# Performance work log

Measured on AMD Instinct MI355X. Metric: run time of the kernel, lower is better.

Reference implementation:

```python
import jax, jax.numpy as jnp
import numpy as np

B, C, H, W = 16, 192, 64, 64
L = 256           # number of quantization levels (len(sos.unique_values))
EXTREMA = 10.0    # codebook support roughly [-extrema, extrema]


def setup_inputs() -> dict:
    key = jax.random.key(0)
    k1, k2, k3 = jax.random.split(key, 3)
    inputs = jax.random.normal(k1, (B, C, H, W), dtype=jnp.float32) * 3.0
    means = jax.random.normal(k2, (B, C, H, W), dtype=jnp.float32)
    # sorted codebook of unique quantizer output values (sos.unique_values)
    raw = jax.random.uniform(k3, (L,), dtype=jnp.float32,
                             minval=-EXTREMA, maxval=EXTREMA)
    unique_values = jnp.sort(raw)
    return {"inputs": inputs, "means": means, "unique_values": unique_values}


def _nearest_symbols(v, unique_values):
    # Parallel binary search over the sorted codebook; equivalent to the
    # original per-element argmin(|keys - x|) in transform_map.
    L_ = unique_values.shape[0]
    idx = jnp.searchsorted(unique_values, v)          # in [0, L]
    idx = jnp.clip(idx, 1, L_ - 1)
    left = unique_values[idx - 1]
    right = unique_values[idx]
    # on ties, argmin picks the lower index -> use <=
    return jnp.where(jnp.abs(v - left) <= jnp.abs(v - right), idx - 1, idx)


def reference(inputs, means, unique_values):
    # quantize(mode='symbols'): subtract means, snap to nearest codebook
    # value, map value -> integer symbol via the sorted codebook.
    v = inputs - means
    symbols = _nearest_symbols(v, unique_values)      # int32 [B,C,H,W]
    # dequantize: symbol -> float codebook value (map_cdf_sos), add means.
    dequant = unique_values[symbols] + means          # float32 [B,C,H,W]
    return dequant, symbols
```

## Files before the change

### kernel.cpp

```cpp
#include <hip/hip_runtime.h>


#define LVL 256

__global__ __launch_bounds__(256) void agc_quant_kernel(
    const float* __restrict__ inputs,
    const float* __restrict__ means,
    const float* __restrict__ uv,
    float* __restrict__ out_deq,
    float* __restrict__ out_sym,
    int n4, int n)
{
    __shared__ float s_uv[LVL];
    s_uv[threadIdx.x] = uv[threadIdx.x];
    __syncthreads();

    int i = blockIdx.x * blockDim.x + threadIdx.x;
    if (i < n4) {
        float4 in = reinterpret_cast<const float4*>(inputs)[i];
        float4 mn = reinterpret_cast<const float4*>(means)[i];

        float vs[4] = {in.x - mn.x, in.y - mn.y, in.z - mn.z, in.w - mn.w};
        float ms[4] = {mn.x, mn.y, mn.z, mn.w};
        float dq[4], sy[4];

        #pragma unroll
        for (int k = 0; k < 4; ++k) {
            float v = vs[k];
            int lo = 0, hi = LVL;
            #pragma unroll
            for (int s = 0; s < 8; ++s) {
                int mid = (lo + hi) >> 1;
                bool go_right = (s_uv[mid] < v);
                lo = go_right ? (mid + 1) : lo;
                hi = go_right ? hi : mid;
            }
            int idx = min(max(lo, 1), LVL - 1);
            float left  = s_uv[idx - 1];
            float right = s_uv[idx];
            bool take_left = (fabsf(v - left) <= fabsf(v - right));
            int   sym = take_left ? (idx - 1) : idx;
            float val = take_left ? left : right;
            dq[k] = val + ms[k];
            sy[k] = (float)sym;
        }

        reinterpret_cast<float4*>(out_deq)[i] = make_float4(dq[0], dq[1], dq[2], dq[3]);
        reinterpret_cast<float4*>(out_sym)[i] = make_float4(sy[0], sy[1], sy[2], sy[3]);
    }

    if (blockIdx.x == 0 && threadIdx.x == 0) {
        for (int j = n4 * 4; j < n; ++j) {
            float m = means[j];
            float v = inputs[j] - m;
            int lo = 0, hi = LVL;
            for (int s = 0; s < 8; ++s) {
                int mid = (lo + hi) >> 1;
                bool go_right = (s_uv[mid] < v);
                lo = go_right ? (mid + 1) : lo;
                hi = go_right ? hi : mid;
            }
            int idx = min(max(lo, 1), LVL - 1);
            float left  = s_uv[idx - 1];
            float right = s_uv[idx];
            bool take_left = (fabsf(v - left) <= fabsf(v - right));
            int   sym = take_left ? (idx - 1) : idx;
            float val = take_left ? left : right;
            out_deq[j] = val + m;
            out_sym[j] = (float)sym;
        }
    }
}

extern "C" void kernel_launch(void* const* d_in, const int* in_sizes, int n_in,
                              void* d_out, int out_size, void* d_ws, size_t ws_size,
                              hipStream_t stream) {
    const float* inputs = (const float*)d_in[0];
    const float* means  = (const float*)d_in[1];
    const float* uv     = (const float*)d_in[2];

    int n  = in_sizes[0];
    int n4 = n / 4;

    float* out     = (float*)d_out;
    float* out_deq = out;
    float* out_sym = out + n;

    int threads = 256;
    int blocks  = (n4 + threads - 1) / threads;
    agc_quant_kernel<<<blocks, threads, 0, stream>>>(
        inputs, means, uv, out_deq, out_sym, n4, n);
}
```

Before: 180.4 us.

## Replace binary search with midpoint bucket lookup table and grid-stride loop

```diff
diff --git a/kernel.cpp b/kernel.cpp
--- a/kernel.cpp
+++ b/kernel.cpp
@@ -1,22 +1,76 @@
 #include <hip/hip_runtime.h>
 
 
-#define LVL 256
+#define LVL   256
+#define NMID  255
+#define MBUCK 4096
+
+
+__global__ __launch_bounds__(256) void agc_build_tables(
+    const float* __restrict__ uv, float* __restrict__ ws)
+{
+    __shared__ float s_uv[LVL];
+    __shared__ float s_mid[NMID];
+
+    int tid = threadIdx.x;
+    s_uv[tid] = uv[tid];
+    __syncthreads();
+
+    if (tid < NMID) {
+        float m = 0.5f * (s_uv[tid] + s_uv[tid + 1]);
+        s_mid[tid] = m;
+        ws[tid] = m;
+    }
+    __syncthreads();
+
+    float lo = s_mid[0];
+    float hi = s_mid[NMID - 1];
+    float scale = (hi > lo) ? ((float)MBUCK / (hi - lo)) : 0.0f;
+    float inv_scale = (hi > lo) ? ((hi - lo) / (float)MBUCK) : 0.0f;
+    if (tid == 0) { ws[256] = lo; ws[257] = scale; }
+
+    int* T = (int*)(ws + 512);
+    for (int m = tid; m < MBUCK; m += 256) {
+        float left = lo + (float)m * inv_scale;
+        int l = 0, h = NMID;
+        #pragma unroll
+        for (int s = 0; s < 8; ++s) {
+            int mid = (l + h) >> 1;
+            bool right = (s_mid[mid] < left);
+            l = right ? (mid + 1) : l;
+            h = right ? h : mid;
+        }
+        int b = l - 1;
+        T[m] = b < 0 ? 0 : b;
+    }
+}
 
 __global__ __launch_bounds__(256) void agc_quant_kernel(
     const float* __restrict__ inputs,
     const float* __restrict__ means,
     const float* __restrict__ uv,
+    const float* __restrict__ ws,
     float* __restrict__ out_deq,
     float* __restrict__ out_sym,
     int n4, int n)
 {
     __shared__ float s_uv[LVL];
-    s_uv[threadIdx.x] = uv[threadIdx.x];
+    __shared__ float s_mid[NMID + 1];
+    __shared__ int   s_T[MBUCK];
+
+    int tid = threadIdx.x;
+    s_uv[tid] = uv[tid];
+    if (tid < NMID) s_mid[tid] = ws[tid];
+    const int* gT = (const int*)(ws + 512);
+    #pragma unroll
+    for (int m = tid; m < MBUCK; m += 256) s_T[m] = gT[m];
+
+    float lo    = ws[256];
+    float scale = ws[257];
     __syncthreads();
 
-    int i = blockIdx.x * blockDim.x + threadIdx.x;
-    if (i < n4) {
+    int stride = gridDim.x * blockDim.x;
+    for (int i = blockIdx.x * blockDim.x + tid; i < n4; i += stride) {
         float4 in = reinterpret_cast<const float4*>(inputs)[i];
         float4 mn = reinterpret_cast<const float4*>(means)[i];
 
@@ -27,47 +81,30 @@
         #pragma unroll
         for (int k = 0; k < 4; ++k) {
             float v = vs[k];
-            int lo = 0, hi = LVL;
-            #pragma unroll
-            for (int s = 0; s < 8; ++s) {
-                int mid = (lo + hi) >> 1;
-                bool go_right = (s_uv[mid] < v);
-                lo = go_right ? (mid + 1) : lo;
-                hi = go_right ? hi : mid;
-            }
-            int idx = min(max(lo, 1), LVL - 1);
-            float left  = s_uv[idx - 1];
-            float right = s_uv[idx];
-            bool take_left = (fabsf(v - left) <= fabsf(v - right));
-            int   sym = take_left ? (idx - 1) : idx;
-            float val = take_left ? left : right;
-            dq[k] = val + ms[k];
-            sy[k] = (float)sym;
+            float f = (v - lo) * scale;
+            int m = (int)f;
+            m = m < 0 ? 0 : (m >= MBUCK ? MBUCK - 1 : m);
+            int base = s_T[m];
+            while (base < NMID && s_mid[base] < v) ++base;
+            sy[k] = (float)base;
+            dq[k] = s_uv[base] + ms[k];
         }
 
         reinterpret_cast<float4*>(out_deq)[i] = make_float4(dq[0], dq[1], dq[2], dq[3]);
         reinterpret_cast<float4*>(out_sym)[i] = make_float4(sy[0], sy[1], sy[2], sy[3]);
     }
 
-    if (blockIdx.x == 0 && threadIdx.x == 0) {
+    if (blockIdx.x == 0 && tid == 0) {
         for (int j = n4 * 4; j < n; ++j) {
-            float m = means[j];
-            float v = inputs[j] - m;
-            int lo = 0, hi = LVL;
-            for (int s = 0; s < 8; ++s) {
-                int mid = (lo + hi) >> 1;
-                bool go_right = (s_uv[mid] < v);
-                lo = go_right ? (mid + 1) : lo;
-                hi = go_right ? hi : mid;
-            }
-            int idx = min(max(lo, 1), LVL - 1);
-            float left  = s_uv[idx - 1];
-            float right = s_uv[idx];
-            bool take_left = (fabsf(v - left) <= fabsf(v - right));
-            int   sym = take_left ? (idx - 1) : idx;
-            float val = take_left ? left : right;
-            out_deq[j] = val + m;
-            out_sym[j] = (float)sym;
+            float mean = means[j];
+            float v = inputs[j] - mean;
+            float f = (v - lo) * scale;
+            int m = (int)f;
+            m = m < 0 ? 0 : (m >= MBUCK ? MBUCK - 1 : m);
+            int base = s_T[m];
+            while (base < NMID && s_mid[base] < v) ++base;
+            out_sym[j] = (float)base;
+            out_deq[j] = s_uv[base] + mean;
         }
     }
 }
@@ -85,9 +122,12 @@
     float* out     = (float*)d_out;
     float* out_deq = out;
     float* out_sym = out + n;
+    float* ws      = (float*)d_ws;
+
+    agc_build_tables<<<1, 256, 0, stream>>>(uv, ws);
 
     int threads = 256;
-    int blocks  = (n4 + threads - 1) / threads;
+    int blocks  = 1536;
     agc_quant_kernel<<<blocks, threads, 0, stream>>>(
-        inputs, means, uv, out_deq, out_sym, n4, n);
+        inputs, means, uv, ws, out_deq, out_sym, n4, n);
 }
```

Result: slower. 190.6 us (+5.7%).

## Replace per-element binary search with bucketed midpoint lookup table

Applied to the files above, without the earlier changes.

```diff
diff --git a/kernel.cpp b/kernel.cpp
--- a/kernel.cpp
+++ b/kernel.cpp
@@ -1,73 +1,156 @@
 #include <hip/hip_runtime.h>
+#include <math.h>
 
 
 #define LVL 256
 
-__global__ __launch_bounds__(256) void agc_quant_kernel(
-    const float* __restrict__ inputs,
-    const float* __restrict__ means,
-    const float* __restrict__ uv,
-    float* __restrict__ out_deq,
-    float* __restrict__ out_sym,
-    int n4, int n)
+__device__ __forceinline__ int lb_bj(const int* s_bj, int x) {
+    int lo = 0, hi = LVL;
+    #pragma unroll
+    for (int s = 0; s < 8; ++s) {
+        int mid = (lo + hi) >> 1;
+        bool r = (s_bj[mid] < x);
+        lo = r ? mid + 1 : lo;
+        hi = r ? hi : mid;
+    }
+    return lo;
+}
+
+__global__ __launch_bounds__(256) void agc_build(
+    const float* __restrict__ uv, float* __restrict__ ws, int NB)
 {
     __shared__ float s_uv[LVL];
-    s_uv[threadIdx.x] = uv[threadIdx.x];
+    __shared__ float s_mid[LVL];
+    __shared__ int   s_bj[LVL];
+    int tid = threadIdx.x;
+    s_uv[tid] = uv[tid];
+    __syncthreads();
+    float mid = (tid < LVL - 1) ? 0.5f * (s_uv[tid] + s_uv[tid + 1]) : INFINITY;
+    s_mid[tid] = mid;
+    __syncthreads();
+    float lo = s_mid[0], hi = s_mid[LVL - 2];
+    float scale = (float)NB / (hi - lo);
+    float f = (mid - lo) * scale;
+    f = fminf(fmaxf(f, 0.0f), (float)(NB - 1));
+    s_bj[tid] = (tid < LVL - 1) ? (int)f : 0x7fffffff;
     __syncthreads();
 
-    int i = blockIdx.x * blockDim.x + threadIdx.x;
-    if (i < n4) {
-        float4 in = reinterpret_cast<const float4*>(inputs)[i];
-        float4 mn = reinterpret_cast<const float4*>(means)[i];
-
-        float vs[4] = {in.x - mn.x, in.y - mn.y, in.z - mn.z, in.w - mn.w};
-        float ms[4] = {mn.x, mn.y, mn.z, mn.w};
-        float dq[4], sy[4];
-
-        #pragma unroll
-        for (int k = 0; k < 4; ++k) {
-            float v = vs[k];
-            int lo = 0, hi = LVL;
-            #pragma unroll
-            for (int s = 0; s < 8; ++s) {
-                int mid = (lo + hi) >> 1;
-                bool go_right = (s_uv[mid] < v);
-                lo = go_right ? (mid + 1) : lo;
-                hi = go_right ? hi : mid;
-            }
-            int idx = min(max(lo, 1), LVL - 1);
-            float left  = s_uv[idx - 1];
-            float right = s_uv[idx];
-            bool take_left = (fabsf(v - left) <= fabsf(v - right));
-            int   sym = take_left ? (idx - 1) : idx;
-            float val = take_left ? left : right;
-            dq[k] = val + ms[k];
-            sy[k] = (float)sym;
-        }
-
-        reinterpret_cast<float4*>(out_deq)[i] = make_float4(dq[0], dq[1], dq[2], dq[3]);
-        reinterpret_cast<float4*>(out_sym)[i] = make_float4(sy[0], sy[1], sy[2], sy[3]);
+    if (blockIdx.x == 0) {
+        float4 p;
+        p.x = s_mid[tid];
+        p.y = s_uv[tid];
+        p.z = (tid < LVL - 1) ? s_uv[tid + 1] : s_uv[LVL - 1];
+        p.w = 0.0f;
+        ((float4*)ws)[tid] = p;
+        if (tid == 0) { ws[1024] = lo; ws[1025] = scale; }
     }
 
-    if (blockIdx.x == 0 && threadIdx.x == 0) {
+    unsigned short* T = (unsigned short*)((char*)ws + 4608);
+    int stride = gridDim.x * blockDim.x;
+    for (int m = blockIdx.x * blockDim.x + tid; m < NB; m += stride) {
+        int l0 = lb_bj(s_bj, m);
+        int l1 = lb_bj(s_bj, m + 1);
+        int cnt = l1 - l0;
+        int base = l0 > 255 ? 255 : l0;
+        int c = cnt > 2 ? 2 : cnt;
+        T[m] = (unsigned short)(base | (c << 8));
+    }
+}
+
+__device__ __forceinline__ int lb_mid(const float4* s_pack, float v) {
+    int lo = 0, hi = LVL;
+    #pragma unroll
+    for (int s = 0; s < 8; ++s) {
+        int mid = (lo + hi) >> 1;
+        bool r = (s_pack[mid].x < v);
+        lo = r ? mid + 1 : lo;
+        hi = r ? hi : mid;
+    }
+    return lo;
+}
+
+__device__ __forceinline__ void agc_one4(
+    const float4& a, const float4& b, const float4* s_pack,
+    const unsigned short* __restrict__ T, float lo, float scale, float fNBm1,
+    float4& dq, float4& sy)
+{
+    float v[4]  = {a.x - b.x, a.y - b.y, a.z - b.z, a.w - b.w};
+    float me[4] = {b.x, b.y, b.z, b.w};
+    float dqs[4], sys[4];
+    int slow = 0;
+    #pragma unroll
+    for (int k = 0; k < 4; ++k) {
+        float f = (v[k] - lo) * scale;
+        f = fminf(fmaxf(f, 0.0f), fNBm1);
+        int e = T[(int)f];
+        int base = e & 255;
+        int c = e >> 8;
+        float4 p = s_pack[base];
+        bool take = (c == 1) && (p.x < v[k]);
+        sys[k] = (float)(base + (take ? 1 : 0));
+        dqs[k] = (take ? p.z : p.y) + me[k];
+        slow |= (c == 2) << k;
+    }
+    if (slow) {
+        #pragma unroll
+        for (int k = 0; k < 4; ++k) if ((slow >> k) & 1) {
+            int s = lb_mid(s_pack, v[k]);
+            sys[k] = (float)s;
+            dqs[k] = s_pack[s].y + me[k];
+        }
+    }
+    dq = make_float4(dqs[0], dqs[1], dqs[2], dqs[3]);
+    sy = make_float4(sys[0], sys[1], sys[2], sys[3]);
+}
+
+__global__ __launch_bounds__(256) void agc_quant(
+    const float* __restrict__ inputs, const float* __restrict__ means,
+    const float* __restrict__ ws, const unsigned short* __restrict__ T,
+    float* __restrict__ out_deq, float* __restrict__ out_sym,
+    int n4, int n, int NB)
+{
+    __shared__ float4 s_pack[LVL];
+    int tid = threadIdx.x;
+    s_pack[tid] = ((const float4*)ws)[tid];
+    float lo = ws[1024], scale = ws[1025];
+    __syncthreads();
+
+    const float4* in4 = (const float4*)inputs;
+    const float4* mn4 = (const float4*)means;
+    float4* dq4 = (float4*)out_deq;
+    float4* sy4 = (float4*)out_sym;
+    float fNBm1 = (float)(NB - 1);
+
+    int i0 = blockIdx.x * 512 + tid;
+    int i1 = i0 + 256;
+
+    if (i1 < n4) {
+        float4 a0 = in4[i0], b0 = mn4[i0], a1 = in4[i1], b1 = mn4[i1];
+        float4 dq0, sy0, dq1, sy1;
+        agc_one4(a0, b0, s_pack, T, lo, scale, fNBm1, dq0, sy0);
+        agc_one4(a1, b1, s_pack, T, lo, scale, fNBm1, dq1, sy1);
+        dq4[i0] = dq0; dq4[i1] = dq1;
+        sy4[i0] = sy0; sy4[i1] = sy1;
+    } else {
+        if (i0 < n4) {
+            float4 a = in4[i0], b = mn4[i0], dq, sy;
+            agc_one4(a, b, s_pack, T, lo, scale, fNBm1, dq, sy);
+            dq4[i0] = dq; sy4[i0] = sy;
+        }
+        if (i1 < n4) {
+            float4 a = in4[i1], b = mn4[i1], dq, sy;
+            agc_one4(a, b, s_pack, T, lo, scale, fNBm1, dq, sy);
+            dq4[i1] = dq; sy4[i1] = sy;
+        }
+    }
+
+    if (blockIdx.x == 0 && tid == 0) {
         for (int j = n4 * 4; j < n; ++j) {
             float m = means[j];
             float v = inputs[j] - m;
-            int lo = 0, hi = LVL;
-            for (int s = 0; s < 8; ++s) {
-                int mid = (lo + hi) >> 1;
-                bool go_right = (s_uv[mid] < v);
-                lo = go_right ? (mid + 1) : lo;
-                hi = go_right ? hi : mid;
-            }
-            int idx = min(max(lo, 1), LVL - 1);
-            float left  = s_uv[idx - 1];
-            float right = s_uv[idx];
-            bool take_left = (fabsf(v - left) <= fabsf(v - right));
-            int   sym = take_left ? (idx - 1) : idx;
-            float val = take_left ? left : right;
-            out_deq[j] = val + m;
-            out_sym[j] = (float)sym;
+            int s = lb_mid(s_pack, v);
+            out_sym[j] = (float)s;
+            out_deq[j] = s_pack[s].y + m;
         }
     }
 }
@@ -85,9 +168,16 @@
     float* out     = (float*)d_out;
     float* out_deq = out;
     float* out_sym = out + n;
+    float* ws      = (float*)d_ws;
 
-    int threads = 256;
-    int blocks  = (n4 + threads - 1) / threads;
-    agc_quant_kernel<<<blocks, threads, 0, stream>>>(
-        inputs, means, uv, out_deq, out_sym, n4, n);
+    long long avail = (long long)ws_size > 4608 ? ((long long)ws_size - 4608) / 2 : 1024;
+    int NB = 1024;
+    while ((long long)NB * 2 <= avail && NB < 32768) NB <<= 1;
+    unsigned short* T = (unsigned short*)((char*)d_ws + 4608);
+
+    agc_build<<<32, 256, 0, stream>>>(uv, ws, NB);
+
+    int blocks = (n4 + 511) / 512;
+    agc_quant<<<blocks, 256, 0, stream>>>(
+        inputs, means, ws, T, out_deq, out_sym, n4, n, NB);
 }
```

After: 220.1 us. 22.0% more time.
